# Kernel optimization log

Hardware: AMD Instinct MI355X
Metric: run time of the kernel (lower is better)

The kernel has to match this reference:

```python
import jax, jax.numpy as jnp
import numpy as np

QUERY_DIM = 1024
KEY_DIM = 1024
NUM_HEADS = 16
HEAD_DIM = QUERY_DIM // NUM_HEADS


def setup_inputs() -> dict:
    key = jax.random.key(0)
    ks = jax.random.split(key, 11)
    B, Sq, Sk = 2, 2048, 2048
    s = 0.02
    return {
        "q": jax.random.normal(ks[0], (B, Sq, QUERY_DIM), jnp.float32),
        "k": jax.random.normal(ks[1], (B, Sk, KEY_DIM), jnp.float32),
        "v": jax.random.normal(ks[2], (B, Sk, KEY_DIM), jnp.float32),
        "Wq": jax.random.normal(ks[3], (QUERY_DIM, QUERY_DIM), jnp.float32) * s,
        "bq": jnp.zeros((QUERY_DIM,), jnp.float32),
        "Wk": jax.random.normal(ks[4], (KEY_DIM, QUERY_DIM), jnp.float32) * s,
        "bk": jnp.zeros((QUERY_DIM,), jnp.float32),
        "Wv": jax.random.normal(ks[5], (KEY_DIM, QUERY_DIM), jnp.float32) * s,
        "bv": jnp.zeros((QUERY_DIM,), jnp.float32),
        "Wo": jax.random.normal(ks[6], (QUERY_DIM, QUERY_DIM), jnp.float32) * s,
        "bo": jnp.zeros((QUERY_DIM,), jnp.float32),
    }


def reference(q, k, v, Wq, bq, Wk, bk, Wv, bv, Wo, bo):
    B, Sq, _ = q.shape
    Sk = k.shape[1]
    scale = HEAD_DIM ** -0.5
    # projections -> [B, H, S, Dh]
    qh = (q @ Wq + bq).reshape(B, Sq, NUM_HEADS, HEAD_DIM).transpose(0, 2, 1, 3)
    kh = (k @ Wk + bk).reshape(B, Sk, NUM_HEADS, HEAD_DIM).transpose(0, 2, 1, 3)
    vh = (v @ Wv + bv).reshape(B, Sk, NUM_HEADS, HEAD_DIM).transpose(0, 2, 1, 3)
    scores = jnp.einsum("bhqd,bhkd->bhqk", qh, kh) * scale
    attn = jax.nn.softmax(scores, axis=-1)
    out = jnp.einsum("bhqk,bhkd->bhqd", attn, vh)
    out = out.transpose(0, 2, 1, 3).reshape(B, Sq, QUERY_DIM)
    return out @ Wo + bo  # dropout is identity at inference
```

## Files before the change

### kernel.cpp

```cpp
#include <hip/hip_runtime.h>
#include <hip/hip_fp16.h>
#include <cstddef>


#define B_   2
#define S_   2048
#define D_   1024
#define H_   16
#define DH_  64

typedef _Float16 half8 __attribute__((ext_vector_type(8)));
typedef _Float16 half4 __attribute__((ext_vector_type(4)));
typedef float floatx4 __attribute__((ext_vector_type(4)));

#define MFMA32(a, b, c) __builtin_amdgcn_mfma_f32_16x16x32_f16((a), (b), (c), 0, 0, 0)
#define MFMA16(a, b, c) __builtin_amdgcn_mfma_f32_16x16x16f16((a), (b), (c), 0, 0, 0)

__global__ __launch_bounds__(256) void prep(
    const float* __restrict__ q, const float* __restrict__ k,
    const float* __restrict__ v,
    __half* __restrict__ qf, __half* __restrict__ kf, __half* __restrict__ vf,
    const float* __restrict__ Wq, const float* __restrict__ Wk,
    const float* __restrict__ Wv, const float* __restrict__ Wo,
    __half* __restrict__ Wtq, __half* __restrict__ Wtk,
    __half* __restrict__ Wtv, __half* __restrict__ Wto)
{
    __shared__ __align__(16) __half T[64][72];
    const int tid = threadIdx.x;
    const int z = blockIdx.z;
    if (z < 3) {
        const float* srcs[3] = {q, k, v};
        __half* dsts[3] = {qf, kf, vf};
        const int i = blockIdx.x * 256 + tid;
        const float4* s = (const float4*)srcs[z];
        const float4 a = s[2 * i], b = s[2 * i + 1];
        half8 h;
        h[0] = (_Float16)a.x; h[1] = (_Float16)a.y; h[2] = (_Float16)a.z; h[3] = (_Float16)a.w;
        h[4] = (_Float16)b.x; h[5] = (_Float16)b.y; h[6] = (_Float16)b.z; h[7] = (_Float16)b.w;
        *(half8*)&dsts[z][(size_t)i * 8] = h;
        return;
    }
    if (blockIdx.x >= 256) return;
    const float* Ws[4] = {Wq, Wk, Wv, Wo};
    __half* Wts[4] = {Wtq, Wtk, Wtv, Wto};
    const int n0 = (blockIdx.x & 15) * 64, k0 = (blockIdx.x >> 4) * 64;
    for (int w = 0; w < 4; ++w) {
        const float* W = Ws[w];
        __half* Wt = Wts[w];
        #pragma unroll
        for (int p = 0; p < 4; ++p) {
            const int c = tid + p * 256;
            const int kr = c >> 4, nc = (c & 15) * 4;
            const float4 a = *(const float4*)&W[(size_t)(k0 + kr) * D_ + n0 + nc];
            T[nc + 0][kr] = __float2half(a.x);
            T[nc + 1][kr] = __float2half(a.y);
            T[nc + 2][kr] = __float2half(a.z);
            T[nc + 3][kr] = __float2half(a.w);
        }
        __syncthreads();
        #pragma unroll
        for (int p = 0; p < 2; ++p) {
            const int c = tid + p * 256;
            const int nr = c >> 3, kc = (c & 7) * 8;
            *(half8*)&Wt[(size_t)(n0 + nr) * D_ + k0 + kc] = *(const half8*)&T[nr][kc];
        }
        __syncthreads();
    }
}

__device__ __forceinline__ void gemm_core(
    const __half* __restrict__ A, const __half* __restrict__ Bt,
    const float* __restrict__ bias, void* __restrict__ dst,
    const int mode, const float oscale)
{
    __shared__ __align__(16) char gsm[36864];
    __half (*As)[72] = (__half(*)[72])gsm;
    __half (*Bs)[72] = (__half(*)[72])(gsm + 18432);

    const int tid = threadIdx.x;
    const int m0 = blockIdx.y * 128, n0 = blockIdx.x * 128;
    const int lane = tid & 63, wv = tid >> 6;
    const int quad = lane >> 4, lr = lane & 15;
    const int wm0 = (wv >> 1) * 64, wn0 = (wv & 1) * 64;

    floatx4 acc[4][4];
    #pragma unroll
    for (int i = 0; i < 4; ++i)
        #pragma unroll
        for (int j = 0; j < 4; ++j)
            acc[i][j] = (floatx4){0.f, 0.f, 0.f, 0.f};

    half8 pa[4], pb[4];
    #pragma unroll
    for (int p = 0; p < 4; ++p) {
        const int c = tid + p * 256;
        const int row = c >> 3, seg = (c & 7) * 8;
        pa[p] = *(const half8*)&A [(size_t)(m0 + row) * D_ + seg];
        pb[p] = *(const half8*)&Bt[(size_t)(n0 + row) * D_ + seg];
    }

    for (int k0 = 0; k0 < D_; k0 += 64) {
        __syncthreads();
        #pragma unroll
        for (int p = 0; p < 4; ++p) {
            const int c = tid + p * 256;
            const int row = c >> 3, seg = (c & 7) * 8;
            *(half8*)&As[row][seg] = pa[p];
            *(half8*)&Bs[row][seg] = pb[p];
        }
        if (k0 + 64 < D_) {
            #pragma unroll
            for (int p = 0; p < 4; ++p) {
                const int c = tid + p * 256;
                const int row = c >> 3, seg = (c & 7) * 8;
                pa[p] = *(const half8*)&A [(size_t)(m0 + row) * D_ + k0 + 64 + seg];
                pb[p] = *(const half8*)&Bt[(size_t)(n0 + row) * D_ + k0 + 64 + seg];
            }
        }
        __syncthreads();
        #pragma unroll
        for (int ks = 0; ks < 2; ++ks) {
            const int ko = quad * 8 + ks * 32;
            half8 af[4], bf[4];
            #pragma unroll
            for (int i = 0; i < 4; ++i) af[i] = *(const half8*)&As[wm0 + i * 16 + lr][ko];
            #pragma unroll
            for (int j = 0; j < 4; ++j) bf[j] = *(const half8*)&Bs[wn0 + j * 16 + lr][ko];
            #pragma unroll
            for (int i = 0; i < 4; ++i)
                #pragma unroll
                for (int j = 0; j < 4; ++j)
                    acc[i][j] = MFMA32(af[i], bf[j], acc[i][j]);
        }
    }

    if (mode == 1) {
        float* out = (float*)dst;
        #pragma unroll
        for (int i = 0; i < 4; ++i) {
            #pragma unroll
            for (int j = 0; j < 4; ++j) {
                const int col = n0 + wn0 + j * 16 + lr;
                const float bval = bias[col];
                #pragma unroll
                for (int r = 0; r < 4; ++r) {
                    const int m = m0 + wm0 + i * 16 + quad * 4 + r;
                    out[(size_t)m * D_ + col] = acc[i][j][r] + bval;
                }
            }
        }
        return;
    }

    __syncthreads();
    __half (*Ct)[136] = (__half(*)[136])gsm;
    #pragma unroll
    for (int i = 0; i < 4; ++i) {
        #pragma unroll
        for (int j = 0; j < 4; ++j) {
            const int nl = wn0 + j * 16 + lr;
            const float bval = bias[n0 + nl];
            #pragma unroll
            for (int r = 0; r < 4; ++r) {
                const int ml = wm0 + i * 16 + quad * 4 + r;
                const _Float16 hv = (_Float16)((acc[i][j][r] + bval) * oscale);
                if (mode == 0) Ct[ml][nl] = hv;
                else           Ct[nl][ml] = hv;
            }
        }
    }
    __syncthreads();
    __half* oh = (__half*)dst;
    #pragma unroll
    for (int p = 0; p < 8; ++p) {
        const int row = (tid >> 4) + p * 16;
        const int cs  = (tid & 15) * 8;
        const half8 vls = *(const half8*)&Ct[row][cs];
        if (mode == 0) {
            const int m = m0 + row, col = n0 + cs;
            const int b = m >> 11, s = m & (S_ - 1);
            const int h = col >> 6, d = col & 63;
            *(half8*)&oh[(((size_t)(b * H_ + h) * S_ + s) << 6) + d] = vls;
        } else {
            const int col = n0 + row, m = m0 + cs;
            const int b = m >> 11, s = m & (S_ - 1);
            const int h = col >> 6, d = col & 63;
            *(half8*)&oh[((size_t)(b * H_ + h) * DH_ + d) * S_ + s] = vls;
        }
    }
}

__global__ __launch_bounds__(256) void gemm_proj(
    const __half* __restrict__ qf, const __half* __restrict__ kf,
    const __half* __restrict__ vf,
    const __half* __restrict__ Wtq, const __half* __restrict__ Wtk,
    const __half* __restrict__ Wtv,
    const float* __restrict__ bq, const float* __restrict__ bk,
    const float* __restrict__ bv,
    __half* __restrict__ qhf, __half* __restrict__ khf, __half* __restrict__ vht)
{
    const __half* As[3] = {qf, kf, vf};
    const __half* Bts[3] = {Wtq, Wtk, Wtv};
    const float* bs[3] = {bq, bk, bv};
    __half* ds[3] = {qhf, khf, vht};
    const int z = blockIdx.z;
    gemm_core(As[z], Bts[z], bs[z], ds[z], z == 2 ? 2 : 0,
              z == 0 ? 0.1803368801111244f : 1.0f);
}

__global__ __launch_bounds__(256) void gemm_final(
    const __half* __restrict__ attf, const __half* __restrict__ Wto,
    const float* __restrict__ bo, float* __restrict__ out)
{
    gemm_core(attf, Wto, bo, out, 1, 1.0f);
}

__global__ __launch_bounds__(256) void attn_f16(
    const __half* __restrict__ qhf, const __half* __restrict__ khf,
    const __half* __restrict__ vht, __half* __restrict__ attf)
{
    __shared__ __align__(16) char smem[36864];

    const int tid = threadIdx.x;
    const int lane = tid & 63, wv = tid >> 6;
    const int quad = lane >> 4, lr = lane & 15;
    const int bh = blockIdx.y;
    const int q0 = blockIdx.x * 64;
    const size_t hbase = (size_t)bh * S_ * DH_;

    half8 qB[4][2];
    #pragma unroll
    for (int qs = 0; qs < 4; ++qs)
        #pragma unroll
        for (int ks = 0; ks < 2; ++ks)
            qB[qs][ks] = *(const half8*)&qhf[hbase
                + (size_t)(q0 + qs * 16 + lr) * DH_ + quad * 8 + ks * 32];

    float lp[4] = {0.f, 0.f, 0.f, 0.f};
    floatx4 O[4][4];
    #pragma unroll
    for (int i = 0; i < 4; ++i)
        #pragma unroll
        for (int j = 0; j < 4; ++j)
            O[i][j] = (floatx4){0.f, 0.f, 0.f, 0.f};

    {
        __half (*K0)[72] = (__half(*)[72])smem;
        __half (*V0)[72] = (__half(*)[72])(smem + 9216);
        #pragma unroll
        for (int p = 0; p < 2; ++p) {
            const int c = tid + p * 256;
            const int row = c >> 3, seg = (c & 7) * 8;
            *(half8*)&K0[row][seg] = *(const half8*)&khf[hbase + (size_t)row * DH_ + seg];
            *(half8*)&V0[row][seg] = *(const half8*)&vht[hbase + (size_t)row * S_ + seg];
        }
    }
    half8 pk[2], pv[2];
    #pragma unroll
    for (int p = 0; p < 2; ++p) {
        const int c = tid + p * 256;
        const int row = c >> 3, seg = (c & 7) * 8;
        pk[p] = *(const half8*)&khf[hbase + (size_t)(64 + row) * DH_ + seg];
        pv[p] = *(const half8*)&vht[hbase + (size_t)row * S_ + 64 + seg];
    }
    __syncthreads();

    for (int kt = 0; kt < S_; kt += 64) {
        const int cb = (kt >> 6) & 1;
        __half (*Ks)[72] = (__half(*)[72])(smem + cb * 18432);
        __half (*Vs)[72] = (__half(*)[72])(smem + cb * 18432 + 9216);
        __half (*Kn)[72] = (__half(*)[72])(smem + (cb ^ 1) * 18432);
        __half (*Vn)[72] = (__half(*)[72])(smem + (cb ^ 1) * 18432 + 9216);

        if (kt + 64 < S_) {
            #pragma unroll
            for (int p = 0; p < 2; ++p) {
                const int c = tid + p * 256;
                const int row = c >> 3, seg = (c & 7) * 8;
                *(half8*)&Kn[row][seg] = pk[p];
                *(half8*)&Vn[row][seg] = pv[p];
            }
            if (kt + 128 < S_) {
                #pragma unroll
                for (int p = 0; p < 2; ++p) {
                    const int c = tid + p * 256;
                    const int row = c >> 3, seg = (c & 7) * 8;
                    pk[p] = *(const half8*)&khf[hbase + (size_t)(kt + 128 + row) * DH_ + seg];
                    pv[p] = *(const half8*)&vht[hbase + (size_t)row * S_ + kt + 128 + seg];
                }
            }
        }

        floatx4 s4[4];
        #pragma unroll
        for (int qs = 0; qs < 4; ++qs) s4[qs] = (floatx4){0.f, 0.f, 0.f, 0.f};
        __builtin_amdgcn_s_setprio(1);
        #pragma unroll
        for (int ks = 0; ks < 2; ++ks) {
            const half8 aK = *(const half8*)&Ks[wv * 16 + lr][quad * 8 + ks * 32];
            #pragma unroll
            for (int qs = 0; qs < 4; ++qs)
                s4[qs] = MFMA32(aK, qB[qs][ks], s4[qs]);
        }
        __builtin_amdgcn_s_setprio(0);

        half4 aV[4];
        #pragma unroll
        for (int ds = 0; ds < 4; ++ds)
            aV[ds] = *(const half4*)&Vs[ds * 16 + lr][wv * 16 + quad * 4];

        half4 pB[4];
        #pragma unroll
        for (int qs = 0; qs < 4; ++qs) {
            #pragma unroll
            for (int r = 0; r < 4; ++r) {
                const float p = __builtin_amdgcn_exp2f(s4[qs][r]);
                lp[qs] += p;
                pB[qs][r] = (_Float16)p;
            }
        }

        __builtin_amdgcn_s_setprio(1);
        #pragma unroll
        for (int ds = 0; ds < 4; ++ds)
            #pragma unroll
            for (int qs = 0; qs < 4; ++qs)
                O[ds][qs] = MFMA16(aV[ds], pB[qs], O[ds][qs]);
        __builtin_amdgcn_s_setprio(0);

        __syncthreads();
    }

    float* L    = (float*)(smem + 17408);
    float* invL = (float*)(smem + 21504);
    float (*R)[68] = (float(*)[68])smem;
    __half (*F)[72] = (__half(*)[72])(smem + 22016);

    #pragma unroll
    for (int qs = 0; qs < 4; ++qs)
        L[(wv * 4 + quad) * 64 + qs * 16 + lr] = lp[qs];
    __syncthreads();
    if (tid < 64) {
        float s = 0.f;
        #pragma unroll
        for (int i = 0; i < 16; ++i) s += L[i * 64 + tid];
        invL[tid] = 1.0f / s;
    }
    __syncthreads();

    const int qc = tid & 63, dg = tid >> 6;
    const float il = invL[qc];

    #pragma unroll
    for (int ds = 0; ds < 4; ++ds) {
        __syncthreads();
        #pragma unroll
        for (int qs = 0; qs < 4; ++qs)
            #pragma unroll
            for (int r = 0; r < 4; ++r)
                R[wv * 16 + quad * 4 + r][qs * 16 + lr] = O[ds][qs][r];
        __syncthreads();
        half4 hv;
        #pragma unroll
        for (int rr = 0; rr < 4; ++rr) {
            const int row = dg * 4 + rr;
            const float v = R[row][qc] + R[16 + row][qc] + R[32 + row][qc] + R[48 + row][qc];
            hv[rr] = (_Float16)(v * il);
        }
        *(half4*)&F[qc][ds * 16 + dg * 4] = hv;
    }
    __syncthreads();

    const int b = bh >> 4, h = bh & 15;
    const int qrow = tid >> 2, dseg = (tid & 3) * 16;
    __half* dstp = &attf[(((size_t)(b * S_ + q0 + qrow)) << 10) + h * DH_ + dseg];
    *(half8*)&dstp[0] = *(const half8*)&F[qrow][dseg];
    *(half8*)&dstp[8] = *(const half8*)&F[qrow][dseg + 8];
}

extern "C" void kernel_launch(void* const* d_in, const int* in_sizes, int n_in,
                              void* d_out, int out_size, void* d_ws, size_t ws_size,
                              hipStream_t stream) {
    const float* q  = (const float*)d_in[0];
    const float* k  = (const float*)d_in[1];
    const float* v  = (const float*)d_in[2];
    const float* Wq = (const float*)d_in[3];
    const float* bq = (const float*)d_in[4];
    const float* Wk = (const float*)d_in[5];
    const float* bk = (const float*)d_in[6];
    const float* Wv = (const float*)d_in[7];
    const float* bv = (const float*)d_in[8];
    const float* Wo = (const float*)d_in[9];
    const float* bo = (const float*)d_in[10];
    float* out = (float*)d_out;

    __half* ws = (__half*)d_ws;
    const size_t NE = (size_t)B_ * S_ * D_;
    __half* qf   = ws;
    __half* kf   = ws + NE;
    __half* vf   = ws + 2 * NE;
    __half* qhf  = ws + 3 * NE;
    __half* khf  = ws + 4 * NE;
    __half* vht  = ws + 5 * NE;
    __half* attf = ws + 6 * NE;
    __half* Wtq  = ws + 7 * NE;
    __half* Wtk  = Wtq + (size_t)D_ * D_;
    __half* Wtv  = Wtk + (size_t)D_ * D_;
    __half* Wto  = Wtv + (size_t)D_ * D_;

    const dim3 blk(256);
    prep<<<dim3((unsigned)(NE / 8 / 256), 1, 4), blk, 0, stream>>>(
        q, k, v, qf, kf, vf, Wq, Wk, Wv, Wo, Wtq, Wtk, Wtv, Wto);

    gemm_proj<<<dim3(D_ / 128, (B_ * S_) / 128, 3), blk, 0, stream>>>(
        qf, kf, vf, Wtq, Wtk, Wtv, bq, bk, bv, qhf, khf, vht);

    attn_f16<<<dim3(S_ / 64, B_ * H_), blk, 0, stream>>>(qhf, khf, vht, attf);

    gemm_final<<<dim3(D_ / 128, (B_ * S_) / 128), blk, 0, stream>>>(attf, Wto, bo, out);
}
```

Baseline: 239.7 us.

## Switch attention core to 32x32x16 MFMA with 2x2 wave tiling and cheaper epilogue

Restructures the attention kernel so each wave computes a 32-key by 32-query score tile with 32x32x16 MFMA instead of several 16x16 MFMAs, splitting waves as 2 key-groups by 2 query-groups. The probabilities are repacked with cvt_pkrtz and a permlane32 swap (or shuffle fallback) so they can feed the PV MFMA directly. The cross-wave reduction in the epilogue shrinks from four-way with several barrier rounds to a single two-way LDS exchange. It also adds a minimum-occupancy launch bound. Register pressure and the lane-swap overhead are the risks.

Result: faster. 229.6 us (-4.2%).

```diff
diff --git a/kernel.cpp b/kernel.cpp
--- a/kernel.cpp
+++ b/kernel.cpp
@@ -12,9 +12,24 @@
 typedef _Float16 half8 __attribute__((ext_vector_type(8)));
 typedef _Float16 half4 __attribute__((ext_vector_type(4)));
 typedef float floatx4 __attribute__((ext_vector_type(4)));
+typedef float floatx16 __attribute__((ext_vector_type(16)));
+typedef int intx4 __attribute__((ext_vector_type(4)));
 
 #define MFMA32(a, b, c) __builtin_amdgcn_mfma_f32_16x16x32_f16((a), (b), (c), 0, 0, 0)
-#define MFMA16(a, b, c) __builtin_amdgcn_mfma_f32_16x16x16f16((a), (b), (c), 0, 0, 0)
+#define MFMA3216(a, b, c) __builtin_amdgcn_mfma_f32_32x32x16_f16((a), (b), (c), 0, 0, 0)
+
+__device__ __forceinline__ void half_swap(int& a, int& b, const int hi) {
+#if __has_builtin(__builtin_amdgcn_permlane32_swap)
+    (void)hi;
+    auto r = __builtin_amdgcn_permlane32_swap(a, b, false, false);
+    a = r[0]; b = r[1];
+#else
+    const int ax = __shfl_xor(a, 32, 64), bx = __shfl_xor(b, 32, 64);
+    const int na = hi ? bx : a;
+    b = hi ? b : ax;
+    a = na;
+#endif
+}
 
 __global__ __launch_bounds__(256) void prep(
     const float* __restrict__ q, const float* __restrict__ k,
@@ -215,7 +230,7 @@
     gemm_core(attf, Wto, bo, out, 1, 1.0f);
 }
 
-__global__ __launch_bounds__(256) void attn_f16(
+__global__ __launch_bounds__(256, 4) void attn_f16(
     const __half* __restrict__ qhf, const __half* __restrict__ khf,
     const __half* __restrict__ vht, __half* __restrict__ attf)
 {
@@ -223,26 +238,22 @@
 
     const int tid = threadIdx.x;
     const int lane = tid & 63, wv = tid >> 6;
-    const int quad = lane >> 4, lr = lane & 15;
+    const int l31 = lane & 31, hi = lane >> 5;
+    const int kb = wv >> 1, qb = wv & 1;
     const int bh = blockIdx.y;
     const int q0 = blockIdx.x * 64;
     const size_t hbase = (size_t)bh * S_ * DH_;
 
-    half8 qB[4][2];
-    #pragma unroll
-    for (int qs = 0; qs < 4; ++qs)
-        #pragma unroll
-        for (int ks = 0; ks < 2; ++ks)
-            qB[qs][ks] = *(const half8*)&qhf[hbase
-                + (size_t)(q0 + qs * 16 + lr) * DH_ + quad * 8 + ks * 32];
-
-    float lp[4] = {0.f, 0.f, 0.f, 0.f};
-    floatx4 O[4][4];
-    #pragma unroll
-    for (int i = 0; i < 4; ++i)
-        #pragma unroll
-        for (int j = 0; j < 4; ++j)
-            O[i][j] = (floatx4){0.f, 0.f, 0.f, 0.f};
+    half8 qB[4];
+    #pragma unroll
+    for (int ds = 0; ds < 4; ++ds)
+        qB[ds] = *(const half8*)&qhf[hbase
+            + (size_t)(q0 + qb * 32 + l31) * DH_ + ds * 16 + hi * 8];
+
+    float lp = 0.f;
+    floatx16 O[2];
+    #pragma unroll
+    for (int i = 0; i < 16; ++i) { O[0][i] = 0.f; O[1][i] = 0.f; }
 
     {
         __half (*K0)[72] = (__half(*)[72])smem;
@@ -291,83 +302,76 @@
             }
         }
 
-        floatx4 s4[4];
-        #pragma unroll
-        for (int qs = 0; qs < 4; ++qs) s4[qs] = (floatx4){0.f, 0.f, 0.f, 0.f};
+        floatx16 s;
+        #pragma unroll
+        for (int i = 0; i < 16; ++i) s[i] = 0.f;
         __builtin_amdgcn_s_setprio(1);
         #pragma unroll
+        for (int ds = 0; ds < 4; ++ds) {
+            const half8 aK = *(const half8*)&Ks[kb * 32 + l31][ds * 16 + hi * 8];
+            s = MFMA3216(aK, qB[ds], s);
+        }
+        __builtin_amdgcn_s_setprio(0);
+
+        #pragma unroll
+        for (int r = 0; r < 16; ++r) {
+            const float e = __builtin_amdgcn_exp2f(s[r]);
+            lp += e;
+            s[r] = e;
+        }
+
+        half8 pB[2];
+        #pragma unroll
         for (int ks = 0; ks < 2; ++ks) {
-            const half8 aK = *(const half8*)&Ks[wv * 16 + lr][quad * 8 + ks * 32];
-            #pragma unroll
-            for (int qs = 0; qs < 4; ++qs)
-                s4[qs] = MFMA32(aK, qB[qs][ks], s4[qs]);
-        }
+            int P0 = __builtin_bit_cast(int, __builtin_amdgcn_cvt_pkrtz(s[ks * 8 + 0], s[ks * 8 + 1]));
+            int P1 = __builtin_bit_cast(int, __builtin_amdgcn_cvt_pkrtz(s[ks * 8 + 2], s[ks * 8 + 3]));
+            int P2 = __builtin_bit_cast(int, __builtin_amdgcn_cvt_pkrtz(s[ks * 8 + 4], s[ks * 8 + 5]));
+            int P3 = __builtin_bit_cast(int, __builtin_amdgcn_cvt_pkrtz(s[ks * 8 + 6], s[ks * 8 + 7]));
+            half_swap(P0, P2, hi);
+            half_swap(P1, P3, hi);
+            const intx4 w = {P0, P1, P2, P3};
+            pB[ks] = __builtin_bit_cast(half8, w);
+        }
+
+        __builtin_amdgcn_s_setprio(1);
+        #pragma unroll
+        for (int db = 0; db < 2; ++db)
+            #pragma unroll
+            for (int ks = 0; ks < 2; ++ks) {
+                const half8 aV = *(const half8*)&Vs[db * 32 + l31][kb * 32 + ks * 16 + hi * 8];
+                O[db] = MFMA3216(aV, pB[ks], O[db]);
+            }
         __builtin_amdgcn_s_setprio(0);
 
-        half4 aV[4];
-        #pragma unroll
-        for (int ds = 0; ds < 4; ++ds)
-            aV[ds] = *(const half4*)&Vs[ds * 16 + lr][wv * 16 + quad * 4];
-
-        half4 pB[4];
-        #pragma unroll
-        for (int qs = 0; qs < 4; ++qs) {
-            #pragma unroll
-            for (int r = 0; r < 4; ++r) {
-                const float p = __builtin_amdgcn_exp2f(s4[qs][r]);
-                lp[qs] += p;
-                pB[qs][r] = (_Float16)p;
-            }
-        }
-
-        __builtin_amdgcn_s_setprio(1);
-        #pragma unroll
-        for (int ds = 0; ds < 4; ++ds)
-            #pragma unroll
-            for (int qs = 0; qs < 4; ++qs)
-                O[ds][qs] = MFMA16(aV[ds], pB[qs], O[ds][qs]);
-        __builtin_amdgcn_s_setprio(0);
-
         __syncthreads();
     }
 
-    float* L    = (float*)(smem + 17408);
-    float* invL = (float*)(smem + 21504);
     float (*R)[68] = (float(*)[68])smem;
-    __half (*F)[72] = (__half(*)[72])(smem + 22016);
-
-    #pragma unroll
-    for (int qs = 0; qs < 4; ++qs)
-        L[(wv * 4 + quad) * 64 + qs * 16 + lr] = lp[qs];
+    __half (*F)[72] = (__half(*)[72])(smem + 17408);
+    float* Lred = (float*)(smem + 26624);
+
+    lp += __shfl_xor(lp, 32, 64);
+    if (lane < 32) Lred[kb * 64 + qb * 32 + l31] = lp;
+    if (kb == 1) {
+        #pragma unroll
+        for (int db = 0; db < 2; ++db)
+            #pragma unroll
+            for (int r = 0; r < 16; ++r) {
+                const int d = db * 32 + (r & 3) + 8 * (r >> 2) + 4 * hi;
+                R[d][qb * 32 + l31] = O[db][r];
+            }
+    }
     __syncthreads();
-    if (tid < 64) {
-        float s = 0.f;
-        #pragma unroll
-        for (int i = 0; i < 16; ++i) s += L[i * 64 + tid];
-        invL[tid] = 1.0f / s;
-    }
-    __syncthreads();
-
-    const int qc = tid & 63, dg = tid >> 6;
-    const float il = invL[qc];
-
-    #pragma unroll
-    for (int ds = 0; ds < 4; ++ds) {
-        __syncthreads();
-        #pragma unroll
-        for (int qs = 0; qs < 4; ++qs)
-            #pragma unroll
-            for (int r = 0; r < 4; ++r)
-                R[wv * 16 + quad * 4 + r][qs * 16 + lr] = O[ds][qs][r];
-        __syncthreads();
-        half4 hv;
-        #pragma unroll
-        for (int rr = 0; rr < 4; ++rr) {
-            const int row = dg * 4 + rr;
-            const float v = R[row][qc] + R[16 + row][qc] + R[32 + row][qc] + R[48 + row][qc];
-            hv[rr] = (_Float16)(v * il);
-        }
-        *(half4*)&F[qc][ds * 16 + dg * 4] = hv;
+    if (kb == 0) {
+        const int qg = qb * 32 + l31;
+        const float il = 1.0f / (Lred[qg] + Lred[64 + qg]);
+        #pragma unroll
+        for (int db = 0; db < 2; ++db)
+            #pragma unroll
+            for (int r = 0; r < 16; ++r) {
+                const int d = db * 32 + (r & 3) + 8 * (r >> 2) + 4 * hi;
+                F[qg][d] = __float2half((O[db][r] + R[d][qg]) * il);
+            }
     }
     __syncthreads();
 
```
